# Kernel tuning notes

Measured on AMD Instinct MI355X. Metric: run time of the kernel, lower is better.

The kernel has to match this reference:

```python
import jax, jax.numpy as jnp
import numpy as np

B, N, D, NH, HID = 64, 197, 768, 8, 3072
LN_EPS = 1e-5

def _ln(x, g, b):
    m = x.mean(-1, keepdims=True)
    v = x.var(-1, keepdims=True)
    return (x - m) / jnp.sqrt(v + LN_EPS) * g + b

def _so8_gate(x, w, bias, scale, eps):
    # x: [B,N,Dg]; eps: [B,N,8 heads,4 planes]. Closed-form SO(8) planar rotations
    # (equivalent to matrix_exp of the 4 sparse 2x2-block generators, composed).
    Bb, Nn, Dg = x.shape
    hd = Dg // 8
    xp = x @ w.T + bias                      # orth_monitor Linear
    xh = xp.reshape(Bb, Nn, 8, hd)           # [B,N,H,hd]
    x8 = xh[..., :8]                         # first 8 channels per head
    ang = eps * scale                        # angles = randn * rotation_scale
    c, s = jnp.cos(ang), jnp.sin(ang)        # [B,N,8,4]
    ev, od = x8[..., 0::2], x8[..., 1::2]    # plane components
    rot8 = jnp.stack([ev * c - od * s, ev * s + od * c], -1).reshape(Bb, Nn, 8, 8)
    rotated = jnp.concatenate([rot8, xh[..., 8:]], -1)
    err = jnp.linalg.norm(rot8 - x8, axis=-1).mean(-1)  # fro norm per head, mean over heads -> [B,N]
    return rotated.reshape(Bb, Nn, Dg) + x, err

def _adapter(x, w, bias, scale, ln_g, ln_b, eps):
    y, err = _so8_gate(x, w, bias, scale, eps)
    return _ln(y, ln_g, ln_b) + x, err

def setup_inputs():
    key = jax.random.key(0)
    ks = jax.random.split(key, 26)
    rn = lambda k, shp, s=0.02: (jax.random.normal(k, shp) * s).astype(jnp.float32)
    z = lambda shp: jnp.zeros(shp, jnp.float32)
    o = lambda shp: jnp.ones(shp, jnp.float32)
    return {
        'x': jax.random.normal(ks[0], (B, N, D), jnp.float32),
        'qkv_w': rn(ks[1], (3 * D, D)), 'qkv_b': z((3 * D,)),
        'proj_w': rn(ks[2], (D, D)), 'proj_b': z((D,)),
        'norm1_g': o((D,)), 'norm1_b': z((D,)),
        'norm2_g': o((D,)), 'norm2_b': z((D,)),
        'orth_w_a': rn(ks[3], (D, D)), 'orth_b_a': z((D,)),
        'scale_a': o((1,)), 'ln_g_a': o((D,)), 'ln_b_a': z((D,)),
        'orth_w_m': rn(ks[4], (HID, HID)), 'orth_b_m': z((HID,)),
        'scale_m': o((1,)), 'ln_g_m': o((HID,)), 'ln_b_m': z((HID,)),
        'fc1_w': rn(ks[5], (HID, D)), 'fc1_b': z((HID,)),
        'fc2_w': rn(ks[6], (D, HID)), 'fc2_b': z((D,)),
        'eps_a': jax.random.normal(ks[7], (B, N, 8, 4), jnp.float32),
        'eps_m': jax.random.normal(ks[8], (B, N, 8, 4), jnp.float32),
    }

def reference(x, qkv_w, qkv_b, proj_w, proj_b, norm1_g, norm1_b, norm2_g, norm2_b,
              orth_w_a, orth_b_a, scale_a, ln_g_a, ln_b_a,
              orth_w_m, orth_b_m, scale_m, ln_g_m, ln_b_m,
              fc1_w, fc1_b, fc2_w, fc2_b, eps_a, eps_m):
    hd = D // NH
    # attention branch
    x1 = _ln(x, norm1_g, norm1_b)
    qkv = (x1 @ qkv_w.T + qkv_b).reshape(B, N, 3, NH, hd).transpose(2, 0, 3, 1, 4)
    q, k, v = qkv[0], qkv[1], qkv[2]
    attn = jax.nn.softmax(jnp.einsum('bhqd,bhkd->bhqk', q, k) * hd ** -0.5, -1)
    ctx = jnp.einsum('bhqk,bhkd->bhqd', attn, v).transpose(0, 2, 1, 3).reshape(B, N, D)
    ctx = ctx @ proj_w.T + proj_b
    xa, e1 = _adapter(ctx, orth_w_a, orth_b_a, scale_a, ln_g_a, ln_b_a, eps_a)
    x = x + xa
    # mlp branch with SO(8) adapter on hidden
    x2 = _ln(x, norm2_g, norm2_b)
    h = jax.nn.gelu(x2 @ fc1_w.T + fc1_b, approximate=False)
    h, e2 = _adapter(h, orth_w_m, orth_b_m, scale_m, ln_g_m, ln_b_m, eps_m)
    xm = h @ fc2_w.T + fc2_b
    x = x + xm
    return x, e1 + e2
```

## Files before the change

### kernel.cpp

```cpp
#include <hip/hip_runtime.h>
#include <hip/hip_bf16.h>
#include <math.h>

#define MROWS (64*197)
#define DMODEL 768
#define DHID   3072

typedef __hip_bfloat16 bf16;
using bf16x8 = __attribute__((ext_vector_type(8))) short;
using f32x4  = __attribute__((ext_vector_type(4))) float;

__device__ __forceinline__ float b2f(bf16 v) { return __bfloat162float(v); }
__device__ __forceinline__ short f2bs(float f) {
    bf16 h = __float2bfloat16(f);
    return *reinterpret_cast<short*>(&h);
}
__device__ __forceinline__ void b8f(bf16x8 v, float* f) {
#pragma unroll
    for (int j = 0; j < 8; ++j)
        f[j] = __uint_as_float(((unsigned int)(unsigned short)v[j]) << 16);
}
__device__ __forceinline__ bf16x8 f8b(const float* f) {
    bf16x8 r;
#pragma unroll
    for (int j = 0; j < 8; ++j) r[j] = f2bs(f[j]);
    return r;
}
__device__ __forceinline__ float gelu_exact(float v) {
    return 0.5f * v * (1.0f + erff(v * 0.70710678118654752f));
}
__device__ __forceinline__ void st1(bf16* p, float v) { *p = __float2bfloat16(v); }
__device__ __forceinline__ void st1(float* p, float v) { *p = v; }

__device__ __forceinline__ void gl_lds16(const short* g, short* l) {
    __builtin_amdgcn_global_load_lds(
        (const __attribute__((address_space(1))) void*)g,
        (__attribute__((address_space(3))) void*)l, 16, 0, 0);
}

__global__ __launch_bounds__(256) void cvt_all_kernel(
        const float* __restrict__ s0, const float* __restrict__ s1,
        const float* __restrict__ s2, const float* __restrict__ s3,
        const float* __restrict__ s4, const float* __restrict__ s5,
        short* __restrict__ dst) {
    const int b0 = 442368, b1 = 589824, b2 = 737280,
              b3 = 3096576, b4 = 3686400, b5 = 4276224;
    int i = blockIdx.x * 256 + threadIdx.x;
    if (i >= b5) return;
    const float* src; int off;
    if      (i < b0) { src = s0; off = i; }
    else if (i < b1) { src = s1; off = i - b0; }
    else if (i < b2) { src = s2; off = i - b1; }
    else if (i < b3) { src = s3; off = i - b2; }
    else if (i < b4) { src = s4; off = i - b3; }
    else             { src = s5; off = i - b4; }
    float4 v = ((const float4*)src)[off];
    ((short4*)dst)[i] = make_short4(f2bs(v.x), f2bs(v.y), f2bs(v.z), f2bs(v.w));
}

__global__ __launch_bounds__(256) void ln1_kernel(const float* __restrict__ in,
        const float* __restrict__ g, const float* __restrict__ b,
        bf16* __restrict__ out, int Dg) {
    int row = blockIdx.x;
    int n4 = Dg >> 2;
    const float4* xr = (const float4*)(in + (size_t)row * Dg);
    float s = 0.f, s2 = 0.f;
    for (int c = threadIdx.x; c < n4; c += 256) {
        float4 v = xr[c];
        s += v.x + v.y + v.z + v.w;
        s2 += v.x * v.x + v.y * v.y + v.z * v.z + v.w * v.w;
    }
    __shared__ float r1[4], r2[4];
    for (int off = 32; off; off >>= 1) { s += __shfl_down(s, off, 64); s2 += __shfl_down(s2, off, 64); }
    if ((threadIdx.x & 63) == 0) { r1[threadIdx.x >> 6] = s; r2[threadIdx.x >> 6] = s2; }
    __syncthreads();
    s  = r1[0] + r1[1] + r1[2] + r1[3];
    s2 = r2[0] + r2[1] + r2[2] + r2[3];
    float mean = s / Dg;
    float rstd = rsqrtf(s2 / Dg - mean * mean + 1e-5f);
    short4* yr = (short4*)(out + (size_t)row * Dg);
    const float4* g4 = (const float4*)g;
    const float4* b4 = (const float4*)b;
    for (int c = threadIdx.x; c < n4; c += 256) {
        float4 v = xr[c], gg = g4[c], bb = b4[c];
        yr[c] = make_short4(f2bs((v.x - mean) * rstd * gg.x + bb.x),
                            f2bs((v.y - mean) * rstd * gg.y + bb.y),
                            f2bs((v.z - mean) * rstd * gg.z + bb.z),
                            f2bs((v.w - mean) * rstd * gg.w + bb.w));
    }
}

template<int MODE, typename TC>
__global__ __launch_bounds__(256) void gemm_bf(const short* __restrict__ A,
        const short* __restrict__ W, const float* __restrict__ bias,
        const bf16* __restrict__ resid, TC* __restrict__ C,
        int Mr, int Nc, int Kc)
{
    __shared__ short Abuf[128 * 64];
    __shared__ short Bbuf[128 * 64];
    const int tid  = threadIdx.x;
    const int lane = tid & 63, wave = tid >> 6;
    const int wm = wave & 1, wn = wave >> 1;
    const int quad = lane >> 4, l16 = lane & 15;
    const int m0 = blockIdx.y * 128, n0 = blockIdx.x * 128;

    f32x4 acc[4][4];
#pragma unroll
    for (int i = 0; i < 4; ++i)
#pragma unroll
        for (int j = 0; j < 4; ++j) acc[i][j] = (f32x4){0.f, 0.f, 0.f, 0.f};

    for (int k0 = 0; k0 < Kc; k0 += 64) {
        __syncthreads();
#pragma unroll
        for (int q = 0; q < 4; ++q) {
            int c = q * 256 + tid;
            int row = c >> 3;
            int j = (c & 7) ^ (row & 7);
            int rowA = m0 + row;
            if (rowA > Mr - 1) rowA = Mr - 1;
            gl_lds16(A + (size_t)rowA * Kc + k0 + j * 8, Abuf + c * 8);
        }
#pragma unroll
        for (int q = 0; q < 4; ++q) {
            int c = q * 256 + tid;
            int row = c >> 3;
            int j = (c & 7) ^ (row & 7);
            gl_lds16(W + (size_t)(n0 + row) * Kc + k0 + j * 8, Bbuf + c * 8);
        }
        __syncthreads();
#pragma unroll
        for (int t = 0; t < 2; ++t) {
            bf16x8 fa[4], fb[4];
#pragma unroll
            for (int i = 0; i < 4; ++i) {
                int r = wm * 64 + i * 16 + l16;
                fa[i] = *(const bf16x8*)(Abuf + r * 64 + (((t * 4 + quad) ^ (r & 7)) << 3));
            }
#pragma unroll
            for (int j = 0; j < 4; ++j) {
                int r = wn * 64 + j * 16 + l16;
                fb[j] = *(const bf16x8*)(Bbuf + r * 64 + (((t * 4 + quad) ^ (r & 7)) << 3));
            }
#pragma unroll
            for (int i = 0; i < 4; ++i)
#pragma unroll
                for (int j = 0; j < 4; ++j)
                    acc[i][j] = __builtin_amdgcn_mfma_f32_16x16x32_bf16(fa[i], fb[j], acc[i][j], 0, 0, 0);
        }
    }

#pragma unroll
    for (int i = 0; i < 4; ++i)
#pragma unroll
        for (int r = 0; r < 4; ++r) {
            int row = m0 + wm * 64 + i * 16 + quad * 4 + r;
            if (row >= Mr) continue;
#pragma unroll
            for (int j = 0; j < 4; ++j) {
                int col = n0 + wn * 64 + j * 16 + l16;
                float v = acc[i][j][r] + bias[col];
                if (MODE == 1) v = gelu_exact(v);
                if (MODE == 2) v += b2f(resid[(size_t)row * Nc + col]);
                st1(C + (size_t)row * Nc + col, v);
            }
        }
}

template<int MODE, typename TC>
__global__ __launch_bounds__(256) void gemm_f32b(const short* __restrict__ A,
        const float* __restrict__ W, const float* __restrict__ bias,
        const bf16* __restrict__ resid, TC* __restrict__ C,
        int Mr, int Nc, int Kc)
{
    __shared__ short Abuf[128 * 32];
    __shared__ short Bbuf[128 * 32];
    const int tid  = threadIdx.x;
    const int lane = tid & 63, wave = tid >> 6;
    const int wm = wave & 1, wn = wave >> 1;
    const int quad = lane >> 4, l16 = lane & 15;
    const int m0 = blockIdx.y * 128, n0 = blockIdx.x * 128;
    f32x4 acc[4][4];
#pragma unroll
    for (int i = 0; i < 4; ++i)
#pragma unroll
        for (int j = 0; j < 4; ++j) acc[i][j] = (f32x4){0.f, 0.f, 0.f, 0.f};
    const int brow = tid >> 3;
    const int bk   = (tid & 7) * 4;
    for (int k0 = 0; k0 < Kc; k0 += 32) {
        float4 wv[4];
#pragma unroll
        for (int s = 0; s < 4; ++s)
            wv[s] = *(const float4*)(W + (size_t)(n0 + s * 32 + brow) * Kc + k0 + bk);
        __syncthreads();
#pragma unroll
        for (int q = 0; q < 2; ++q) {
            int c = q * 256 + tid;
            int rowA = m0 + (c >> 2);
            if (rowA > Mr - 1) rowA = Mr - 1;
            gl_lds16(A + (size_t)rowA * Kc + k0 + (c & 3) * 8, Abuf + c * 8);
        }
#pragma unroll
        for (int s = 0; s < 4; ++s) {
            short4 h = make_short4(f2bs(wv[s].x), f2bs(wv[s].y), f2bs(wv[s].z), f2bs(wv[s].w));
            *(short4*)(Bbuf + (s * 32 + brow) * 32 + bk) = h;
        }
        __syncthreads();
        bf16x8 fa[4], fb[4];
#pragma unroll
        for (int i = 0; i < 4; ++i)
            fa[i] = *(const bf16x8*)(Abuf + (wm * 64 + i * 16 + l16) * 32 + quad * 8);
#pragma unroll
        for (int j = 0; j < 4; ++j)
            fb[j] = *(const bf16x8*)(Bbuf + (wn * 64 + j * 16 + l16) * 32 + quad * 8);
#pragma unroll
        for (int i = 0; i < 4; ++i)
#pragma unroll
            for (int j = 0; j < 4; ++j)
                acc[i][j] = __builtin_amdgcn_mfma_f32_16x16x32_bf16(fa[i], fb[j], acc[i][j], 0, 0, 0);
    }
#pragma unroll
    for (int i = 0; i < 4; ++i)
#pragma unroll
        for (int r = 0; r < 4; ++r) {
            int row = m0 + wm * 64 + i * 16 + quad * 4 + r;
            if (row >= Mr) continue;
#pragma unroll
            for (int j = 0; j < 4; ++j) {
                int col = n0 + wn * 64 + j * 16 + l16;
                float v = acc[i][j][r] + bias[col];
                if (MODE == 1) v = gelu_exact(v);
                if (MODE == 2) v += b2f(resid[(size_t)row * Nc + col]);
                st1(C + (size_t)row * Nc + col, v);
            }
        }
}

__global__ __launch_bounds__(256) void attn_mfma(const bf16* __restrict__ qkv,
        bf16* __restrict__ ctx) {
    const int NS = 197;
    const int KST = 104;
    const int VST = 232;
    __shared__ short Kbuf[224 * KST];
    __shared__ short Vt[96 * VST];
    __shared__ short Pbuf[4][16 * VST];
    const int b = blockIdx.x >> 3, h = blockIdx.x & 7;
    const short* base = (const short*)qkv + (size_t)b * NS * 2304 + h * 96;
    const int tid = threadIdx.x;

    for (int c = tid; c < NS * 12; c += 256) {
        int key = c / 12, dc = c % 12;
        bf16x8 v = *(const bf16x8*)(base + (size_t)key * 2304 + 768 + dc * 8);
        *(bf16x8*)(Kbuf + key * KST + dc * 8) = v;
    }
    for (int c = tid; c < 27 * 12; c += 256) {
        int key = NS + c / 12, dc = c % 12;
        *(bf16x8*)(Kbuf + key * KST + dc * 8) = (bf16x8){0, 0, 0, 0, 0, 0, 0, 0};
    }
    for (int c = tid; c < NS * 12; c += 256) {
        int key = c / 12, dc = c % 12;
        bf16x8 v = *(const bf16x8*)(base + (size_t)key * 2304 + 1536 + dc * 8);
#pragma unroll
        for (int j = 0; j < 8; ++j) Vt[(dc * 8 + j) * VST + key] = v[j];
    }
    for (int c = tid; c < 96 * 27; c += 256) {
        int d = c / 27, key = NS + c % 27;
        Vt[d * VST + key] = 0;
    }
    __syncthreads();

    const int wave = tid >> 6, lane = tid & 63;
    const int quad = lane >> 4, l16 = lane & 15;
    short* P = &Pbuf[wave][0];

    for (int qt = wave; qt < 13; qt += 4) {
        int qrow = qt * 16 + l16; if (qrow > NS - 1) qrow = NS - 1;
        bf16x8 fq[3];
#pragma unroll
        for (int kc = 0; kc < 3; ++kc)
            fq[kc] = *(const bf16x8*)(base + (size_t)qrow * 2304 + kc * 32 + quad * 8);
        f32x4 s[14];
#pragma unroll
        for (int nt = 0; nt < 14; ++nt) {
            s[nt] = (f32x4){0.f, 0.f, 0.f, 0.f};
#pragma unroll
            for (int kc = 0; kc < 3; ++kc) {
                bf16x8 fk = *(const bf16x8*)(Kbuf + (nt * 16 + l16) * KST + kc * 32 + quad * 8);
                s[nt] = __builtin_amdgcn_mfma_f32_16x16x32_bf16(fq[kc], fk, s[nt], 0, 0, 0);
            }
        }
        const float sc = 0.10206207261596577f;
        float mx[4] = {-1e30f, -1e30f, -1e30f, -1e30f};
#pragma unroll
        for (int nt = 0; nt < 14; ++nt) {
            bool valid = nt * 16 + l16 < NS;
#pragma unroll
            for (int r = 0; r < 4; ++r) {
                float v = s[nt][r] * sc;
                s[nt][r] = v;
                if (valid) mx[r] = fmaxf(mx[r], v);
            }
        }
#pragma unroll
        for (int m = 1; m < 16; m <<= 1)
#pragma unroll
            for (int r = 0; r < 4; ++r) mx[r] = fmaxf(mx[r], __shfl_xor(mx[r], m, 64));
        float l[4] = {0.f, 0.f, 0.f, 0.f};
#pragma unroll
        for (int nt = 0; nt < 14; ++nt) {
            bool valid = nt * 16 + l16 < NS;
#pragma unroll
            for (int r = 0; r < 4; ++r) {
                float e = valid ? __expf(s[nt][r] - mx[r]) : 0.f;
                l[r] += e;
                P[(quad * 4 + r) * VST + nt * 16 + l16] = f2bs(e);
            }
        }
#pragma unroll
        for (int m = 1; m < 16; m <<= 1)
#pragma unroll
            for (int r = 0; r < 4; ++r) l[r] += __shfl_xor(l[r], m, 64);
        __asm__ volatile("s_waitcnt lgkmcnt(0)" ::: "memory");
        f32x4 o[6];
#pragma unroll
        for (int nt = 0; nt < 6; ++nt) o[nt] = (f32x4){0.f, 0.f, 0.f, 0.f};
#pragma unroll
        for (int kc = 0; kc < 7; ++kc) {
            bf16x8 fp = *(const bf16x8*)(P + l16 * VST + kc * 32 + quad * 8);
#pragma unroll
            for (int nt = 0; nt < 6; ++nt) {
                bf16x8 fv = *(const bf16x8*)(Vt + (nt * 16 + l16) * VST + kc * 32 + quad * 8);
                o[nt] = __builtin_amdgcn_mfma_f32_16x16x32_bf16(fp, fv, o[nt], 0, 0, 0);
            }
        }
        float inv[4];
#pragma unroll
        for (int r = 0; r < 4; ++r) inv[r] = 1.f / l[r];
#pragma unroll
        for (int r = 0; r < 4; ++r) {
            int q = qt * 16 + quad * 4 + r;
            if (q >= NS) continue;
            bf16* orow = ctx + ((size_t)(b * NS + q)) * 768 + h * 96;
#pragma unroll
            for (int nt = 0; nt < 6; ++nt)
                orow[nt * 16 + l16] = __float2bfloat16(o[nt][r] * inv[r]);
        }
    }
}

template<bool OUTER, bool FINAL, bool FLN2>
__global__ __launch_bounds__(256) void adapter_finish(
        const bf16* __restrict__ xp, const bf16* __restrict__ xin,
        const float* __restrict__ xouter, const float* __restrict__ eps,
        const float* __restrict__ scale_p, const float* __restrict__ g,
        const float* __restrict__ bta, bf16* __restrict__ out,
        float* __restrict__ e_acc, float* __restrict__ e_out,
        const float* __restrict__ g2, const float* __restrict__ b2,
        bf16* __restrict__ out2, int Dg)
{
    extern __shared__ float smem[];
    float* y = smem;
    float* diff2 = smem + Dg;
    float* red = diff2 + 64;
    float* r1 = red + 8;
    float* r2 = red + 12;
    int row = blockIdx.x;
    int hd = Dg >> 3;
    int hd8 = hd >> 3;
    int n8 = Dg >> 3;
    const bf16* xpr = xp + (size_t)row * Dg;
    const bf16* xir = xin + (size_t)row * Dg;
    int tid = threadIdx.x;
    if (tid < 64) {
        int hh = tid >> 3, i = tid & 7, p = i >> 1;
        float ang = eps[((size_t)row * 8 + hh) * 4 + p] * scale_p[0];
        float c = cosf(ang), sn = sinf(ang);
        int base = hh * hd;
        float ev = b2f(xpr[base + 2 * p]), od = b2f(xpr[base + 2 * p + 1]);
        float r = (i & 1) ? (ev * sn + od * c) : (ev * c - od * sn);
        float d = r - b2f(xpr[base + i]);
        diff2[tid] = d * d;
        y[base + i] = r + b2f(xir[base + i]);
    }
    for (int c8 = tid; c8 < n8; c8 += 256) {
        if (c8 % hd8 == 0) continue;
        float a[8], bvx[8];
        b8f(*(const bf16x8*)(xpr + c8 * 8), a);
        b8f(*(const bf16x8*)(xir + c8 * 8), bvx);
#pragma unroll
        for (int j = 0; j < 8; ++j) y[c8 * 8 + j] = a[j] + bvx[j];
    }
    __syncthreads();
    if (tid < 8) {
        float t = 0.f;
#pragma unroll
        for (int i = 0; i < 8; ++i) t += diff2[tid * 8 + i];
        red[tid] = sqrtf(t);
    }
    float s = 0.f, s2 = 0.f;
    for (int c = tid; c < Dg; c += 256) { float v = y[c]; s += v; s2 += v * v; }
    for (int off = 32; off; off >>= 1) { s += __shfl_down(s, off, 64); s2 += __shfl_down(s2, off, 64); }
    if ((tid & 63) == 0) { r1[tid >> 6] = s; r2[tid >> 6] = s2; }
    __syncthreads();
    s  = r1[0] + r1[1] + r1[2] + r1[3];
    s2 = r2[0] + r2[1] + r2[2] + r2[3];
    float mean = s / Dg;
    float rstd = rsqrtf(s2 / Dg - mean * mean + 1e-5f);
    if (tid == 0) {
        float e = (red[0] + red[1] + red[2] + red[3] + red[4] + red[5] + red[6] + red[7]) * 0.125f;
        if (FINAL) e_out[row] = e_acc[row] + e;
        else       e_acc[row] = e;
    }
    bf16* outr = out + (size_t)row * Dg;
    const float4* g4 = (const float4*)g;
    const float4* bt4 = (const float4*)bta;
    const float4* xo4 = OUTER ? (const float4*)(xouter + (size_t)row * Dg) : nullptr;
    float sB = 0.f, sB2 = 0.f;
    for (int c8 = tid; c8 < n8; c8 += 256) {
        float xi[8];
        b8f(*(const bf16x8*)(xir + c8 * 8), xi);
        float4 gg0 = g4[c8 * 2], gg1 = g4[c8 * 2 + 1];
        float4 bb0 = bt4[c8 * 2], bb1 = bt4[c8 * 2 + 1];
        float gv[8] = {gg0.x, gg0.y, gg0.z, gg0.w, gg1.x, gg1.y, gg1.z, gg1.w};
        float bv[8] = {bb0.x, bb0.y, bb0.z, bb0.w, bb1.x, bb1.y, bb1.z, bb1.w};
        float vv[8];
#pragma unroll
        for (int j = 0; j < 8; ++j)
            vv[j] = (y[c8 * 8 + j] - mean) * rstd * gv[j] + bv[j] + xi[j];
        if (OUTER) {
            float4 o0 = xo4[c8 * 2], o1 = xo4[c8 * 2 + 1];
            float ov[8] = {o0.x, o0.y, o0.z, o0.w, o1.x, o1.y, o1.z, o1.w};
#pragma unroll
            for (int j = 0; j < 8; ++j) vv[j] += ov[j];
        }
        *(bf16x8*)(outr + c8 * 8) = f8b(vv);
        if (FLN2) {
#pragma unroll
            for (int j = 0; j < 8; ++j) {
                y[c8 * 8 + j] = vv[j];
                sB += vv[j]; sB2 += vv[j] * vv[j];
            }
        }
    }
    if (FLN2) {
        __syncthreads();
        for (int off = 32; off; off >>= 1) { sB += __shfl_down(sB, off, 64); sB2 += __shfl_down(sB2, off, 64); }
        if ((tid & 63) == 0) { r1[tid >> 6] = sB; r2[tid >> 6] = sB2; }
        __syncthreads();
        sB  = r1[0] + r1[1] + r1[2] + r1[3];
        sB2 = r2[0] + r2[1] + r2[2] + r2[3];
        float mean2 = sB / Dg;
        float rstd2 = rsqrtf(sB2 / Dg - mean2 * mean2 + 1e-5f);
        bf16* o2r = out2 + (size_t)row * Dg;
        const float4* g24 = (const float4*)g2;
        const float4* b24 = (const float4*)b2;
        for (int c8 = tid; c8 < n8; c8 += 256) {
            float4 gg0 = g24[c8 * 2], gg1 = g24[c8 * 2 + 1];
            float4 bb0 = b24[c8 * 2], bb1 = b24[c8 * 2 + 1];
            float gv[8] = {gg0.x, gg0.y, gg0.z, gg0.w, gg1.x, gg1.y, gg1.z, gg1.w};
            float bv[8] = {bb0.x, bb0.y, bb0.z, bb0.w, bb1.x, bb1.y, bb1.z, bb1.w};
            float vv[8];
#pragma unroll
            for (int j = 0; j < 8; ++j)
                vv[j] = (y[c8 * 8 + j] - mean2) * rstd2 * gv[j] + bv[j];
            *(bf16x8*)(o2r + c8 * 8) = f8b(vv);
        }
    }
}

extern "C" void kernel_launch(void* const* d_in, const int* in_sizes, int n_in,
                              void* d_out, int out_size, void* d_ws, size_t ws_size,
                              hipStream_t stream) {
    (void)in_sizes; (void)n_in; (void)out_size;
    const int M = MROWS;
    const size_t S_D = (size_t)M * DMODEL;
    const size_t S_H = (size_t)M * DHID;

    const float* x      = (const float*)d_in[0];
    const float* qkv_w  = (const float*)d_in[1];
    const float* qkv_b  = (const float*)d_in[2];
    const float* proj_w = (const float*)d_in[3];
    const float* proj_b = (const float*)d_in[4];
    const float* n1g    = (const float*)d_in[5];
    const float* n1b    = (const float*)d_in[6];
    const float* n2g    = (const float*)d_in[7];
    const float* n2b    = (const float*)d_in[8];
    const float* wa     = (const float*)d_in[9];
    const float* ba     = (const float*)d_in[10];
    const float* sca    = (const float*)d_in[11];
    const float* lga    = (const float*)d_in[12];
    const float* lba    = (const float*)d_in[13];
    const float* wm     = (const float*)d_in[14];
    const float* bm     = (const float*)d_in[15];
    const float* scm    = (const float*)d_in[16];
    const float* lgm    = (const float*)d_in[17];
    const float* lbm    = (const float*)d_in[18];
    const float* f1w    = (const float*)d_in[19];
    const float* f1b    = (const float*)d_in[20];
    const float* f2w    = (const float*)d_in[21];
    const float* f2b    = (const float*)d_in[22];
    const float* eps_a  = (const float*)d_in[23];
    const float* eps_m  = (const float*)d_in[24];

    float* out_x = (float*)d_out;
    float* out_e = out_x + S_D;

    bf16* R1 = (bf16*)d_ws;
    bf16* R2 = R1 + S_H;
    bf16* R3 = R2 + S_H;
    float* E = (float*)(R3 + S_D);

    const size_t n_qkv = (size_t)2304 * 768, n_proj = (size_t)768 * 768,
                 n_wa = (size_t)768 * 768, n_wm = (size_t)3072 * 3072,
                 n_f1 = (size_t)3072 * 768, n_f2 = (size_t)768 * 3072;
    const size_t base_bytes = (2 * S_H + S_D) * 2 + (size_t)M * 4;
    const size_t w_elems = n_qkv + n_proj + n_wa + n_wm + n_f1 + n_f2;
    const bool cache_w = ws_size >= base_bytes + w_elems * 2;

    short* WB    = (short*)((char*)d_ws + base_bytes);
    short* wb_qkv = WB;
    short* wb_proj = wb_qkv + n_qkv;
    short* wb_wa  = wb_proj + n_proj;
    short* wb_wm  = wb_wa + n_wa;
    short* wb_f1  = wb_wm + n_wm;
    short* wb_f2  = wb_f1 + n_f1;

    const int GY = (M + 127) / 128;
    const size_t lds_a = (DMODEL + 96) * sizeof(float);
    const size_t lds_m = (DHID + 96) * sizeof(float);

    if (cache_w) {
        cvt_all_kernel<<<(4276224 + 255) / 256, 256, 0, stream>>>(
            qkv_w, proj_w, wa, wm, f1w, f2w, WB);
        ln1_kernel<<<M, 256, 0, stream>>>(x, n1g, n1b, R1, DMODEL);
        gemm_bf<0, bf16><<<dim3(2304 / 128, GY), 256, 0, stream>>>(
            (const short*)R1, wb_qkv, qkv_b, nullptr, R2, M, 2304, DMODEL);
        attn_mfma<<<64 * 8, 256, 0, stream>>>(R2, R1);
        gemm_bf<0, bf16><<<dim3(DMODEL / 128, GY), 256, 0, stream>>>(
            (const short*)R1, wb_proj, proj_b, nullptr, R2, M, DMODEL, DMODEL);
        gemm_bf<0, bf16><<<dim3(DMODEL / 128, GY), 256, 0, stream>>>(
            (const short*)R2, wb_wa, ba, nullptr, R1, M, DMODEL, DMODEL);
        adapter_finish<true, false, true><<<M, 256, lds_a, stream>>>(
            R1, R2, x, eps_a, sca, lga, lba, R3, E, nullptr, n2g, n2b, R2, DMODEL);
        gemm_bf<1, bf16><<<dim3(DHID / 128, GY), 256, 0, stream>>>(
            (const short*)R2, wb_f1, f1b, nullptr, R1, M, DHID, DMODEL);
        gemm_bf<0, bf16><<<dim3(DHID / 128, GY), 256, 0, stream>>>(
            (const short*)R1, wb_wm, bm, nullptr, R2, M, DHID, DHID);
        adapter_finish<false, true, false><<<M, 256, lds_m, stream>>>(
            R2, R1, nullptr, eps_m, scm, lgm, lbm, R1, E, out_e, nullptr, nullptr, nullptr, DHID);
        gemm_bf<2, float><<<dim3(DMODEL / 128, GY), 256, 0, stream>>>(
            (const short*)R1, wb_f2, f2b, R3, out_x, M, DMODEL, DHID);
    } else {
        ln1_kernel<<<M, 256, 0, stream>>>(x, n1g, n1b, R1, DMODEL);
        gemm_f32b<0, bf16><<<dim3(2304 / 128, GY), 256, 0, stream>>>(
            (const short*)R1, qkv_w, qkv_b, nullptr, R2, M, 2304, DMODEL);
        attn_mfma<<<64 * 8, 256, 0, stream>>>(R2, R1);
        gemm_f32b<0, bf16><<<dim3(DMODEL / 128, GY), 256, 0, stream>>>(
            (const short*)R1, proj_w, proj_b, nullptr, R2, M, DMODEL, DMODEL);
        gemm_f32b<0, bf16><<<dim3(DMODEL / 128, GY), 256, 0, stream>>>(
            (const short*)R2, wa, ba, nullptr, R1, M, DMODEL, DMODEL);
        adapter_finish<true, false, true><<<M, 256, lds_a, stream>>>(
            R1, R2, x, eps_a, sca, lga, lba, R3, E, nullptr, n2g, n2b, R2, DMODEL);
        gemm_f32b<1, bf16><<<dim3(DHID / 128, GY), 256, 0, stream>>>(
            (const short*)R2, f1w, f1b, nullptr, R1, M, DHID, DMODEL);
        gemm_f32b<0, bf16><<<dim3(DHID / 128, GY), 256, 0, stream>>>(
            (const short*)R1, wm, bm, nullptr, R2, M, DHID, DHID);
        adapter_finish<false, true, false><<<M, 256, lds_m, stream>>>(
            R2, R1, nullptr, eps_m, scm, lgm, lbm, R1, E, out_e, nullptr, nullptr, nullptr, DHID);
        gemm_f32b<2, float><<<dim3(DMODEL / 128, GY), 256, 0, stream>>>(
            (const short*)R1, f2w, f2b, R3, out_x, M, DMODEL, DHID);
    }
}
```

Before: 928.4 us.

## Add 256x256 tiled 8-wave GEMM with pipelined LDS staging for large GEMMs

Introduces a new gemm256 kernel with 256x256 output tiles, 512 threads, double-buffered async global-to-LDS loads interleaved with MFMA sub-tiles, XOR-swizzled LDS layout, s_setprio around MFMAs, and XCD-aware block remapping. It replaces the 128x128 GEMM for the QKV, fc1 and the 3072x3072 orth_m GEMMs. The aim is higher arithmetic intensity and better overlap of loads with compute on the dominant GEMMs. The trade-off is 128 KB of LDS per block, very high register pressure from a 32-fragment accumulator, and wasted work on the padded last row tile.

```diff
diff --git a/kernel.cpp b/kernel.cpp
--- a/kernel.cpp
+++ b/kernel.cpp
@@ -88,6 +88,163 @@
                             f2bs((v.z - mean) * rstd * gg.z + bb.z),
                             f2bs((v.w - mean) * rstd * gg.w + bb.w));
     }
+}
+
+
+#define G256_BAR        __builtin_amdgcn_s_barrier()
+#define G256_LGKM0      asm volatile("s_waitcnt lgkmcnt(0)" ::: "memory")
+#define G256_VM6        asm volatile("s_waitcnt vmcnt(6)" ::: "memory")
+#define G256_VM0        asm volatile("s_waitcnt vmcnt(0)" ::: "memory")
+
+#define G256_STAGE_A(BUF, SET, KT) do {                                        \
+    _Pragma("unroll")                                                          \
+    for (int qq = 0; qq < 2; ++qq) {                                           \
+        int rl = qq * 128 + (SET) * 64 + (tid >> 3);                           \
+        int rg = m0 + rl; if (rg > Mr - 1) rg = Mr - 1;                        \
+        int jc = (tid & 7) ^ (rl & 7);                                         \
+        gl_lds16(A + (size_t)rg * Kc + (KT) + jc * 8,                          \
+                 As[BUF] + rl * 64 + (tid & 7) * 8);                           \
+    } } while (0)
+
+#define G256_STAGE_B(BUF, SET, KT) do {                                        \
+    _Pragma("unroll")                                                          \
+    for (int qq = 0; qq < 2; ++qq) {                                           \
+        int rl = (qq * 2 + (tid >> 8)) * 64 + (SET) * 32 + ((tid & 255) >> 3); \
+        int jc = (tid & 7) ^ (rl & 7);                                         \
+        gl_lds16(W + (size_t)(n0 + rl) * Kc + (KT) + jc * 8,                   \
+                 Bs[BUF] + rl * 64 + (tid & 7) * 8);                           \
+    } } while (0)
+
+#define G256_LDA(BUF, MQ) do {                                                 \
+    _Pragma("unroll")                                                          \
+    for (int i = 0; i < 4; ++i) {                                              \
+        int row = wm * 128 + (MQ) * 64 + i * 16 + l16;                         \
+        const short* rp = As[BUF] + row * 64;                                  \
+        _Pragma("unroll")                                                      \
+        for (int ks = 0; ks < 2; ++ks)                                         \
+            a[i][ks] = *(const bf16x8*)(rp + (((ks * 4 + quad) ^ (row & 7)) << 3)); \
+    } } while (0)
+
+#define G256_LDB(BUF, NQ) do {                                                 \
+    _Pragma("unroll")                                                          \
+    for (int j = 0; j < 2; ++j) {                                              \
+        int row = wn * 64 + (NQ) * 32 + j * 16 + l16;                          \
+        const short* rp = Bs[BUF] + row * 64;                                  \
+        _Pragma("unroll")                                                      \
+        for (int ks = 0; ks < 2; ++ks)                                         \
+            b[j][ks] = *(const bf16x8*)(rp + (((ks * 4 + quad) ^ (row & 7)) << 3)); \
+    } } while (0)
+
+#define G256_MMA(MQ, NQ) do {                                                  \
+    __builtin_amdgcn_s_setprio(1);                                             \
+    _Pragma("unroll")                                                          \
+    for (int i = 0; i < 4; ++i)                                                \
+        _Pragma("unroll")                                                      \
+        for (int j = 0; j < 2; ++j)                                            \
+            _Pragma("unroll")                                                  \
+            for (int ks = 0; ks < 2; ++ks)                                     \
+                acc[(MQ) * 4 + i][(NQ) * 2 + j] =                              \
+                    __builtin_amdgcn_mfma_f32_16x16x32_bf16(                   \
+                        a[i][ks], b[j][ks], acc[(MQ) * 4 + i][(NQ) * 2 + j], 0, 0, 0); \
+    __builtin_amdgcn_s_setprio(0);                                             \
+} while (0)
+
+template<int MODE, typename TC>
+__global__ __launch_bounds__(512, 2) void gemm256(const short* __restrict__ A,
+        const short* __restrict__ W, const float* __restrict__ bias,
+        const bf16* __restrict__ resid, TC* __restrict__ C,
+        int Mr, int Nc, int Kc, int ntn)
+{
+    __shared__ short As[2][256 * 64];
+    __shared__ short Bs[2][256 * 64];
+    const int tid  = threadIdx.x;
+    const int lane = tid & 63, wave = tid >> 6;
+    const int wm = wave >> 2, wn = wave & 3;
+    const int quad = lane >> 4, l16 = lane & 15;
+
+    const int nwg = gridDim.x;
+    const int qd = nwg >> 3, rm = nwg & 7;
+    const int xcd = blockIdx.x & 7, lin = blockIdx.x >> 3;
+    const int wg = (xcd < rm ? xcd * (qd + 1) : rm * (qd + 1) + (xcd - rm) * qd) + lin;
+    const int m0 = (wg / ntn) * 256, n0 = (wg % ntn) * 256;
+
+    f32x4 acc[8][4];
+#pragma unroll
+    for (int i = 0; i < 8; ++i)
+#pragma unroll
+        for (int j = 0; j < 4; ++j) acc[i][j] = (f32x4){0.f, 0.f, 0.f, 0.f};
+    bf16x8 a[4][2], b[2][2];
+
+    const int niter = Kc >> 7;
+
+    G256_STAGE_A(0, 0, 0);  G256_STAGE_B(0, 1, 0);
+    G256_STAGE_A(0, 1, 0);  G256_STAGE_B(0, 0, 0);
+    G256_STAGE_A(1, 0, 64); G256_STAGE_B(1, 1, 64); G256_STAGE_A(1, 1, 64);
+    G256_VM6;
+    G256_BAR;
+
+    for (int it = 0; it < niter; ++it) {
+        const int kT = it * 128;
+        const bool pre = (it + 1 < niter);
+        G256_LDA(0, 0); G256_LDB(0, 0);
+        G256_STAGE_B(1, 0, kT + 64);
+        G256_BAR; G256_LGKM0;
+        G256_MMA(0, 0);
+        G256_BAR;
+        G256_LDB(0, 1);
+        if (pre) G256_STAGE_A(0, 0, kT + 128);
+        G256_BAR; G256_LGKM0;
+        G256_MMA(0, 1);
+        G256_BAR;
+        G256_LDA(0, 1);
+        if (pre) G256_STAGE_B(0, 1, kT + 128);
+        G256_BAR; G256_LGKM0;
+        G256_MMA(1, 1);
+        G256_BAR;
+        G256_LDB(0, 0);
+        if (pre) G256_STAGE_A(0, 1, kT + 128);
+        G256_BAR; G256_LGKM0;
+        G256_MMA(1, 0);
+        if (pre) { G256_VM6; } else { G256_VM0; }
+        G256_BAR;
+        G256_LDA(1, 0); G256_LDB(1, 0);
+        if (pre) G256_STAGE_B(0, 0, kT + 128);
+        G256_BAR; G256_LGKM0;
+        G256_MMA(0, 0);
+        G256_BAR;
+        G256_LDB(1, 1);
+        if (pre) G256_STAGE_A(1, 0, kT + 192);
+        G256_BAR; G256_LGKM0;
+        G256_MMA(0, 1);
+        G256_BAR;
+        G256_LDA(1, 1);
+        if (pre) G256_STAGE_B(1, 1, kT + 192);
+        G256_BAR; G256_LGKM0;
+        G256_MMA(1, 1);
+        G256_BAR;
+        G256_LDB(1, 0);
+        if (pre) G256_STAGE_A(1, 1, kT + 192);
+        G256_BAR; G256_LGKM0;
+        G256_MMA(1, 0);
+        G256_VM6;
+        G256_BAR;
+    }
+
+#pragma unroll
+    for (int fm = 0; fm < 8; ++fm)
+#pragma unroll
+        for (int r = 0; r < 4; ++r) {
+            int row = m0 + wm * 128 + fm * 16 + quad * 4 + r;
+            if (row >= Mr) continue;
+#pragma unroll
+            for (int fn = 0; fn < 4; ++fn) {
+                int col = n0 + wn * 64 + fn * 16 + l16;
+                float v = acc[fm][fn][r] + bias[col];
+                if (MODE == 1) v = gelu_exact(v);
+                if (MODE == 2) v += b2f(resid[(size_t)row * Nc + col]);
+                st1(C + (size_t)row * Nc + col, v);
+            }
+        }
 }
 
 template<int MODE, typename TC>
@@ -526,6 +683,7 @@
     short* wb_f2  = wb_f1 + n_f1;
 
     const int GY = (M + 127) / 128;
+    const int GY256 = (M + 255) / 256;
     const size_t lds_a = (DMODEL + 96) * sizeof(float);
     const size_t lds_m = (DHID + 96) * sizeof(float);
 
@@ -533,8 +691,8 @@
         cvt_all_kernel<<<(4276224 + 255) / 256, 256, 0, stream>>>(
             qkv_w, proj_w, wa, wm, f1w, f2w, WB);
         ln1_kernel<<<M, 256, 0, stream>>>(x, n1g, n1b, R1, DMODEL);
-        gemm_bf<0, bf16><<<dim3(2304 / 128, GY), 256, 0, stream>>>(
-            (const short*)R1, wb_qkv, qkv_b, nullptr, R2, M, 2304, DMODEL);
+        gemm256<0, bf16><<<dim3((2304 / 256) * GY256), 512, 0, stream>>>(
+            (const short*)R1, wb_qkv, qkv_b, nullptr, R2, M, 2304, DMODEL, 2304 / 256);
         attn_mfma<<<64 * 8, 256, 0, stream>>>(R2, R1);
         gemm_bf<0, bf16><<<dim3(DMODEL / 128, GY), 256, 0, stream>>>(
             (const short*)R1, wb_proj, proj_b, nullptr, R2, M, DMODEL, DMODEL);
@@ -542,10 +700,10 @@
             (const short*)R2, wb_wa, ba, nullptr, R1, M, DMODEL, DMODEL);
         adapter_finish<true, false, true><<<M, 256, lds_a, stream>>>(
             R1, R2, x, eps_a, sca, lga, lba, R3, E, nullptr, n2g, n2b, R2, DMODEL);
-        gemm_bf<1, bf16><<<dim3(DHID / 128, GY), 256, 0, stream>>>(
-            (const short*)R2, wb_f1, f1b, nullptr, R1, M, DHID, DMODEL);
-        gemm_bf<0, bf16><<<dim3(DHID / 128, GY), 256, 0, stream>>>(
-            (const short*)R1, wb_wm, bm, nullptr, R2, M, DHID, DHID);
+        gemm256<1, bf16><<<dim3((DHID / 256) * GY256), 512, 0, stream>>>(
+            (const short*)R2, wb_f1, f1b, nullptr, R1, M, DHID, DMODEL, DHID / 256);
+        gemm256<0, bf16><<<dim3((DHID / 256) * GY256), 512, 0, stream>>>(
+            (const short*)R1, wb_wm, bm, nullptr, R2, M, DHID, DHID, DHID / 256);
         adapter_finish<false, true, false><<<M, 256, lds_m, stream>>>(
             R2, R1, nullptr, eps_m, scm, lgm, lbm, R1, E, out_e, nullptr, nullptr, nullptr, DHID);
         gemm_bf<2, float><<<dim3(DMODEL / 128, GY), 256, 0, stream>>>(
```

After: 978.6 us. 1.05x slower.
